# Kernel optimization log

Hardware: AMD Instinct MI355X
Metric: run time of the kernel (lower is better)

Reference implementation:

```python
import jax, jax.numpy as jnp
import numpy as np

ALPHA = 0.1  # label smoothing coefficient

def setup_inputs() -> dict:
    key = jax.random.key(0)
    k1, k2, k3 = jax.random.split(key, 3)
    B, T, V = 8, 512, 8192
    inputs = jax.random.normal(k1, (B, T, V), dtype=jnp.float32)
    # token ids in [2, V); last position of every sample is EOS (id 1)
    body = jax.random.randint(k2, (B, T), 2, V)
    targets = body.at[:, -1].set(1)
    matric = jax.random.uniform(k3, (V, V), dtype=jnp.float32)  # confusion matrix
    label_lengths = jnp.full((B,), T - 1, dtype=jnp.int32)  # len(label); target adds EOS
    return {"inputs": inputs, "matric": matric, "targets": targets,
            "label_lengths": label_lengths}


def reference(inputs, matric, targets, label_lengths):
    B, T, V = inputs.shape
    x = inputs.reshape(-1, V)          # [N, V]
    t = targets.reshape(-1)            # [N]
    N = x.shape[0]

    # --- segment-wise confusion lookup (vectorized over ragged segments) ---
    eos = (t == 1)
    # row index for each token: previous token in its segment, or N-1 at a
    # segment start (faithful to `targets.shape[-1]-1` in the source).
    prev = jnp.roll(t, 1)
    is_start = jnp.roll(eos, 1).at[0].set(True)
    forth = jnp.where(is_start, N - 1, prev)
    need_smoothed = matric[forth, t]   # [N]

    # --- per-segment smoothing coefficient, broadcast to tokens ---
    length = label_lengths + 1                                   # [B]
    sm = 1.0 - jnp.power(1.0 - ALPHA, 1.0 / length.astype(jnp.float32))  # [B]
    eos_i = eos.astype(jnp.int32)
    seg_id = jnp.cumsum(eos_i) - eos_i                           # [N] segment index
    smoothing = sm[seg_id] * need_smoothed                       # [N]

    # --- smoothed target distribution ---
    off = smoothing / (V - 1)                                    # off-target mass
    src = 1.0 - off * V                                          # 1 - weight.sum(1)
    weight = jnp.broadcast_to(off[:, None], (N, V))
    weight = weight.at[jnp.arange(N), t].set(src)

    # --- KLDiv(log_softmax(x), weight), reduction='none', then sum/len ---
    logp = jax.nn.log_softmax(x, axis=1)
    kl = jax.scipy.special.xlogy(weight, weight) - weight * logp
    return kl.sum() / length.sum()
```

## Files before the change

kernel.cpp:

```cpp
#include <hip/hip_runtime.h>
#include <math.h>

#define ALPHA 0.1f

__global__ __launch_bounds__(256) void token_params_kernel(
    const int* __restrict__ t, const float* __restrict__ matric,
    const int* __restrict__ lens, float* __restrict__ offv,
    float* __restrict__ srcv, float* __restrict__ lensum,
    int N, int V, int B)
{
    __shared__ int cnts[256];
    const int tid = threadIdx.x;
    const int chunk = (N + 255) / 256;
    const int c0 = tid * chunk;
    const int c1 = min(c0 + chunk, N);

    int cnt = 0;
    for (int n = c0; n < c1; ++n) cnt += (t[n] == 1);
    cnts[tid] = cnt;
    __syncthreads();

    for (int d = 1; d < 256; d <<= 1) {
        int v = 0;
        if (tid >= d) v = cnts[tid - d];
        __syncthreads();
        if (tid >= d) cnts[tid] += v;
        __syncthreads();
    }
    int run = (tid == 0) ? 0 : cnts[tid - 1];

    const float inv_vm1 = 1.0f / (float)(V - 1);
    for (int n = c0; n < c1; ++n) {
        const int tn = t[n];
        const bool e = (tn == 1);
        int seg = run;
        if (e) run += 1;
        seg = min(seg, B - 1);
        if (seg < 0) seg = 0;

        const int prev = (n == 0) ? 0 : t[n - 1];
        const bool is_start = (n == 0) || (prev == 1);
        const int forth = is_start ? (N - 1) : prev;

        const float need = matric[(size_t)forth * V + tn];
        const float len = (float)(lens[seg] + 1);
        const float sm = 1.0f - powf(1.0f - ALPHA, 1.0f / len);
        const float off = sm * need * inv_vm1;
        offv[n] = off;
        srcv[n] = 1.0f - off * (float)V;
    }

    if (tid == 0) {
        float ls = 0.f;
        for (int b = 0; b < B; ++b) ls += (float)(lens[b] + 1);
        lensum[0] = ls;
    }
}

__device__ __forceinline__ void combine_ms(float& m, float& s, float om, float os) {
    float nm = fmaxf(m, om);
    s = s * __expf(m - nm) + os * __expf(om - nm);
    m = nm;
}

__device__ __forceinline__ void row_epilogue(
    float M, float Z, float Sx, float xt,
    const float* __restrict__ offv, const float* __restrict__ srcv,
    float* __restrict__ rowkl, int row, int V)
{
    const float logZ = logf(Z) + M;
    const float lpt = xt - logZ;
    const float S = Sx - (float)V * logZ;
    const float o = offv[row];
    const float sr = srcv[row];
    const float xlo = (o > 0.f) ? o * logf(o) : 0.f;
    const float xls = (sr > 0.f) ? sr * logf(sr) : 0.f;
    rowkl[row] = (float)(V - 1) * xlo + xls - (o * (S - lpt) + sr * lpt);
}

template <int NV4>
__global__ __launch_bounds__(256) void row_kl_kernel(
    const float* __restrict__ x, const int* __restrict__ t,
    const float* __restrict__ offv, const float* __restrict__ srcv,
    float* __restrict__ rowkl, int V)
{
    const int row = blockIdx.x;
    const int tid = threadIdx.x;
    const float4* xr = reinterpret_cast<const float4*>(x + (size_t)row * V);

    float4 v[NV4];
#pragma unroll
    for (int k = 0; k < NV4; ++k) v[k] = xr[tid + k * 256];

    const int tgt = t[row];
    float m = -INFINITY, sx = 0.f, xt_local = 0.f;
    bool have = false;
#pragma unroll
    for (int k = 0; k < NV4; ++k) {
        const float4 q = v[k];
        m = fmaxf(fmaxf(fmaxf(m, q.x), q.y), fmaxf(q.z, q.w));
        sx += (q.x + q.y) + (q.z + q.w);
        const int c = tgt - 4 * (tid + k * 256);
        if (c >= 0 && c < 4) {
            xt_local = (c == 0) ? q.x : (c == 1) ? q.y : (c == 2) ? q.z : q.w;
            have = true;
        }
    }
    float s = 0.f;
#pragma unroll
    for (int k = 0; k < NV4; ++k) {
        const float4 q = v[k];
        s += (__expf(q.x - m) + __expf(q.y - m)) + (__expf(q.z - m) + __expf(q.w - m));
    }

    __shared__ float sm_m[4], sm_s[4], sm_sx[4], sm_xt;
    if (have) sm_xt = xt_local;

    for (int d = 1; d < 64; d <<= 1) {
        float om = __shfl_xor(m, d);
        float os = __shfl_xor(s, d);
        float osx = __shfl_xor(sx, d);
        combine_ms(m, s, om, os);
        sx += osx;
    }
    const int lane = tid & 63, wid = tid >> 6;
    if (lane == 0) { sm_m[wid] = m; sm_s[wid] = s; sm_sx[wid] = sx; }
    __syncthreads();
    if (tid == 0) {
        for (int w = 1; w < 4; ++w) { combine_ms(m, s, sm_m[w], sm_s[w]); sx += sm_sx[w]; }
        row_epilogue(m, s, sx, sm_xt, offv, srcv, rowkl, row, V);
    }
}

__global__ __launch_bounds__(256) void row_kl_generic(
    const float* __restrict__ x, const int* __restrict__ t,
    const float* __restrict__ offv, const float* __restrict__ srcv,
    float* __restrict__ rowkl, int V)
{
    const int row = blockIdx.x;
    const int tid = threadIdx.x;
    const float* xr = x + (size_t)row * V;
    const int tgt = t[row];

    float m = -INFINITY, sx = 0.f, xt = 0.f;
    bool have = false;
    for (int i = tid; i < V; i += 256) {
        const float q = xr[i];
        m = fmaxf(m, q);
        sx += q;
        if (i == tgt) { xt = q; have = true; }
    }
    __shared__ float shm[4], shs[4], shsx[4], shxt, shM;
    if (have) shxt = xt;
    for (int d = 1; d < 64; d <<= 1) {
        m = fmaxf(m, __shfl_xor(m, d));
        sx += __shfl_xor(sx, d);
    }
    const int lane = tid & 63, wid = tid >> 6;
    if (lane == 0) { shm[wid] = m; shsx[wid] = sx; }
    __syncthreads();
    if (tid == 0) {
        float M = shm[0];
        for (int w = 1; w < 4; ++w) M = fmaxf(M, shm[w]);
        shM = M;
    }
    __syncthreads();
    const float M = shM;
    float s = 0.f;
    for (int i = tid; i < V; i += 256) s += __expf(xr[i] - M);
    for (int d = 1; d < 64; d <<= 1) s += __shfl_xor(s, d);
    if (lane == 0) shs[wid] = s;
    __syncthreads();
    if (tid == 0) {
        const float Z = shs[0] + shs[1] + shs[2] + shs[3];
        const float SX = shsx[0] + shsx[1] + shsx[2] + shsx[3];
        row_epilogue(M, Z, SX, shxt, offv, srcv, rowkl, row, V);
    }
}

__global__ __launch_bounds__(256) void finalize_kernel(
    const float* __restrict__ rowkl, const float* __restrict__ lensum,
    float* __restrict__ out, int N)
{
    __shared__ float sh[4];
    float a = 0.f;
    for (int i = threadIdx.x; i < N; i += 256) a += rowkl[i];
    for (int d = 1; d < 64; d <<= 1) a += __shfl_xor(a, d);
    const int lane = threadIdx.x & 63, wid = threadIdx.x >> 6;
    if (lane == 0) sh[wid] = a;
    __syncthreads();
    if (threadIdx.x == 0) {
        out[0] = (sh[0] + sh[1] + sh[2] + sh[3]) / lensum[0];
    }
}

extern "C" void kernel_launch(void* const* d_in, const int* in_sizes, int n_in,
                              void* d_out, int out_size, void* d_ws, size_t ws_size,
                              hipStream_t stream) {
    const float* x      = (const float*)d_in[0];
    const float* matric = (const float*)d_in[1];
    const int*   tgts   = (const int*)d_in[2];
    const int*   lens   = (const int*)d_in[3];

    const int N = in_sizes[2];
    const int B = in_sizes[3];
    const int V = in_sizes[0] / in_sizes[2];

    float* ws     = (float*)d_ws;
    float* rowkl  = ws;
    float* offv   = ws + N;
    float* srcv   = ws + 2 * N;
    float* lensum = ws + 3 * N;

    token_params_kernel<<<1, 256, 0, stream>>>(tgts, matric, lens, offv, srcv,
                                               lensum, N, V, B);
    if (V == 8 * 256 * 4) {
        row_kl_kernel<8><<<N, 256, 0, stream>>>(x, tgts, offv, srcv, rowkl, V);
    } else {
        row_kl_generic<<<N, 256, 0, stream>>>(x, tgts, offv, srcv, rowkl, V);
    }
    finalize_kernel<<<1, 256, 0, stream>>>(rowkl, lensum, (float*)d_out, N);
}
```

Measured before the change: 400.6 us.

## Fuse per-token parameter computation and final reduction into row KL kernel

For the specialized vocabulary size, the single-block token-parameter kernel and the finalize kernel are removed. Each row block now counts EOS tokens before its row to find its segment, looks up the confusion entry itself, and atomically adds its scaled KL term to the output, which a one-thread kernel zeroes first. This removes a serial one-block kernel and a reduction launch. In exchange every block rescans up to N targets (a quadratic amount of small reads overall) and the atomic float sum has nondeterministic ordering.

After: 396.5 us. Within noise of the previous version (-1.0%).

```diff
diff --git a/kernel.cpp b/kernel.cpp
--- a/kernel.cpp
+++ b/kernel.cpp
@@ -3,58 +3,8 @@
 
 #define ALPHA 0.1f
 
-__global__ __launch_bounds__(256) void token_params_kernel(
-    const int* __restrict__ t, const float* __restrict__ matric,
-    const int* __restrict__ lens, float* __restrict__ offv,
-    float* __restrict__ srcv, float* __restrict__ lensum,
-    int N, int V, int B)
-{
-    __shared__ int cnts[256];
-    const int tid = threadIdx.x;
-    const int chunk = (N + 255) / 256;
-    const int c0 = tid * chunk;
-    const int c1 = min(c0 + chunk, N);
-
-    int cnt = 0;
-    for (int n = c0; n < c1; ++n) cnt += (t[n] == 1);
-    cnts[tid] = cnt;
-    __syncthreads();
-
-    for (int d = 1; d < 256; d <<= 1) {
-        int v = 0;
-        if (tid >= d) v = cnts[tid - d];
-        __syncthreads();
-        if (tid >= d) cnts[tid] += v;
-        __syncthreads();
-    }
-    int run = (tid == 0) ? 0 : cnts[tid - 1];
-
-    const float inv_vm1 = 1.0f / (float)(V - 1);
-    for (int n = c0; n < c1; ++n) {
-        const int tn = t[n];
-        const bool e = (tn == 1);
-        int seg = run;
-        if (e) run += 1;
-        seg = min(seg, B - 1);
-        if (seg < 0) seg = 0;
-
-        const int prev = (n == 0) ? 0 : t[n - 1];
-        const bool is_start = (n == 0) || (prev == 1);
-        const int forth = is_start ? (N - 1) : prev;
-
-        const float need = matric[(size_t)forth * V + tn];
-        const float len = (float)(lens[seg] + 1);
-        const float sm = 1.0f - powf(1.0f - ALPHA, 1.0f / len);
-        const float off = sm * need * inv_vm1;
-        offv[n] = off;
-        srcv[n] = 1.0f - off * (float)V;
-    }
-
-    if (tid == 0) {
-        float ls = 0.f;
-        for (int b = 0; b < B; ++b) ls += (float)(lens[b] + 1);
-        lensum[0] = ls;
-    }
+__global__ void zero_out_kernel(float* __restrict__ out) {
+    out[0] = 0.0f;
 }
 
 __device__ __forceinline__ void combine_ms(float& m, float& s, float om, float os) {
@@ -63,34 +13,48 @@
     m = nm;
 }
 
-__device__ __forceinline__ void row_epilogue(
-    float M, float Z, float Sx, float xt,
-    const float* __restrict__ offv, const float* __restrict__ srcv,
-    float* __restrict__ rowkl, int row, int V)
-{
-    const float logZ = logf(Z) + M;
-    const float lpt = xt - logZ;
-    const float S = Sx - (float)V * logZ;
-    const float o = offv[row];
-    const float sr = srcv[row];
-    const float xlo = (o > 0.f) ? o * logf(o) : 0.f;
-    const float xls = (sr > 0.f) ? sr * logf(sr) : 0.f;
-    rowkl[row] = (float)(V - 1) * xlo + xls - (o * (S - lpt) + sr * lpt);
-}
-
 template <int NV4>
-__global__ __launch_bounds__(256) void row_kl_kernel(
-    const float* __restrict__ x, const int* __restrict__ t,
-    const float* __restrict__ offv, const float* __restrict__ srcv,
-    float* __restrict__ rowkl, int V)
+__global__ __launch_bounds__(256) void fused_row_kl(
+    const float* __restrict__ x, const float* __restrict__ matric,
+    const int* __restrict__ t, const int* __restrict__ lens,
+    float* __restrict__ out, int N, int V, int B)
 {
     const int row = blockIdx.x;
     const int tid = threadIdx.x;
+
     const float4* xr = reinterpret_cast<const float4*>(x + (size_t)row * V);
-
     float4 v[NV4];
 #pragma unroll
     for (int k = 0; k < NV4; ++k) v[k] = xr[tid + k * 256];
+
+    int cnt = 0;
+    for (int i = tid; i < row; i += 256) cnt += (t[i] == 1);
+    for (int d = 1; d < 64; d <<= 1) cnt += __shfl_xor(cnt, d);
+
+    __shared__ int scnt[4];
+    __shared__ float sh_off, sh_src, sh_ls, sh_xt;
+    __shared__ float sm_m[4], sm_s[4], sm_sx[4];
+    const int lane = tid & 63, wid = tid >> 6;
+    if (lane == 0) scnt[wid] = cnt;
+    __syncthreads();
+
+    if (tid == 0) {
+        int seg = scnt[0] + scnt[1] + scnt[2] + scnt[3];
+        seg = min(max(seg, 0), B - 1);
+        const int tn = t[row];
+        const int prev = (row == 0) ? 0 : t[row - 1];
+        const bool is_start = (row == 0) || (prev == 1);
+        const int forth = is_start ? (N - 1) : prev;
+        const float need = matric[(size_t)forth * V + tn];
+        const float len = (float)(lens[seg] + 1);
+        const float sm = 1.0f - powf(1.0f - ALPHA, 1.0f / len);
+        const float off = sm * need / (float)(V - 1);
+        sh_off = off;
+        sh_src = 1.0f - off * (float)V;
+        float ls = 0.f;
+        for (int b = 0; b < B; ++b) ls += (float)(lens[b] + 1);
+        sh_ls = ls;
+    }
 
     const int tgt = t[row];
     float m = -INFINITY, sx = 0.f, xt_local = 0.f;
@@ -106,15 +70,14 @@
             have = true;
         }
     }
+    if (have) sh_xt = xt_local;
+
     float s = 0.f;
 #pragma unroll
     for (int k = 0; k < NV4; ++k) {
         const float4 q = v[k];
         s += (__expf(q.x - m) + __expf(q.y - m)) + (__expf(q.z - m) + __expf(q.w - m));
     }
-
-    __shared__ float sm_m[4], sm_s[4], sm_sx[4], sm_xt;
-    if (have) sm_xt = xt_local;
 
     for (int d = 1; d < 64; d <<= 1) {
         float om = __shfl_xor(m, d);
@@ -123,12 +86,67 @@
         combine_ms(m, s, om, os);
         sx += osx;
     }
-    const int lane = tid & 63, wid = tid >> 6;
     if (lane == 0) { sm_m[wid] = m; sm_s[wid] = s; sm_sx[wid] = sx; }
     __syncthreads();
+
     if (tid == 0) {
         for (int w = 1; w < 4; ++w) { combine_ms(m, s, sm_m[w], sm_s[w]); sx += sm_sx[w]; }
-        row_epilogue(m, s, sx, sm_xt, offv, srcv, rowkl, row, V);
+        const float logZ = logf(s) + m;
+        const float lpt = sh_xt - logZ;
+        const float S = sx - (float)V * logZ;
+        const float o = sh_off;
+        const float sr = sh_src;
+        const float xlo = (o > 0.f) ? o * logf(o) : 0.f;
+        const float xls = (sr > 0.f) ? sr * logf(sr) : 0.f;
+        const float kl = (float)(V - 1) * xlo + xls - (o * (S - lpt) + sr * lpt);
+        atomicAdd(out, kl / sh_ls);
+    }
+}
+
+__global__ __launch_bounds__(256) void token_params_kernel(
+    const int* __restrict__ t, const float* __restrict__ matric,
+    const int* __restrict__ lens, float* __restrict__ offv,
+    float* __restrict__ srcv, float* __restrict__ lensum,
+    int N, int V, int B)
+{
+    __shared__ int cnts[256];
+    const int tid = threadIdx.x;
+    const int chunk = (N + 255) / 256;
+    const int c0 = tid * chunk;
+    const int c1 = min(c0 + chunk, N);
+
+    int cnt = 0;
+    for (int n = c0; n < c1; ++n) cnt += (t[n] == 1);
+    cnts[tid] = cnt;
+    __syncthreads();
+    for (int d = 1; d < 256; d <<= 1) {
+        int v = 0;
+        if (tid >= d) v = cnts[tid - d];
+        __syncthreads();
+        if (tid >= d) cnts[tid] += v;
+        __syncthreads();
+    }
+    int run = (tid == 0) ? 0 : cnts[tid - 1];
+
+    const float inv_vm1 = 1.0f / (float)(V - 1);
+    for (int n = c0; n < c1; ++n) {
+        const int tn = t[n];
+        int seg = min(max(run, 0), B - 1);
+        if (tn == 1) run += 1;
+        const int prev = (n == 0) ? 0 : t[n - 1];
+        const bool is_start = (n == 0) || (prev == 1);
+        const int forth = is_start ? (N - 1) : prev;
+        const float need = matric[(size_t)forth * V + tn];
+        const float len = (float)(lens[seg] + 1);
+        const float sm = 1.0f - powf(1.0f - ALPHA, 1.0f / len);
+        const float off = sm * need * inv_vm1;
+        offv[n] = off;
+        srcv[n] = 1.0f - off * (float)V;
+    }
+    if (tid == 0) {
+        float ls = 0.f;
+        for (int b = 0; b < B; ++b) ls += (float)(lens[b] + 1);
+        lensum[0] = ls;
     }
 }
 
@@ -174,7 +192,14 @@
     if (tid == 0) {
         const float Z = shs[0] + shs[1] + shs[2] + shs[3];
         const float SX = shsx[0] + shsx[1] + shsx[2] + shsx[3];
-        row_epilogue(M, Z, SX, shxt, offv, srcv, rowkl, row, V);
+        const float logZ = logf(Z) + M;
+        const float lpt = shxt - logZ;
+        const float S = SX - (float)V * logZ;
+        const float o = offv[row];
+        const float sr = srcv[row];
+        const float xlo = (o > 0.f) ? o * logf(o) : 0.f;
+        const float xls = (sr > 0.f) ? sr * logf(sr) : 0.f;
+        rowkl[row] = (float)(V - 1) * xlo + xls - (o * (S - lpt) + sr * lpt);
     }
 }
 
@@ -206,18 +231,19 @@
     const int B = in_sizes[3];
     const int V = in_sizes[0] / in_sizes[2];
 
-    float* ws     = (float*)d_ws;
-    float* rowkl  = ws;
-    float* offv   = ws + N;
-    float* srcv   = ws + 2 * N;
-    float* lensum = ws + 3 * N;
-
-    token_params_kernel<<<1, 256, 0, stream>>>(tgts, matric, lens, offv, srcv,
-                                               lensum, N, V, B);
     if (V == 8 * 256 * 4) {
-        row_kl_kernel<8><<<N, 256, 0, stream>>>(x, tgts, offv, srcv, rowkl, V);
+        zero_out_kernel<<<1, 1, 0, stream>>>((float*)d_out);
+        fused_row_kl<8><<<N, 256, 0, stream>>>(x, matric, tgts, lens,
+                                               (float*)d_out, N, V, B);
     } else {
+        float* ws     = (float*)d_ws;
+        float* rowkl  = ws;
+        float* offv   = ws + N;
+        float* srcv   = ws + 2 * N;
+        float* lensum = ws + 3 * N;
+        token_params_kernel<<<1, 256, 0, stream>>>(tgts, matric, lens, offv, srcv,
+                                                   lensum, N, V, B);
         row_kl_generic<<<N, 256, 0, stream>>>(x, tgts, offv, srcv, rowkl, V);
-    }
-    finalize_kernel<<<1, 256, 0, stream>>>(rowkl, lensum, (float*)d_out, N);
-}
+        finalize_kernel<<<1, 256, 0, stream>>>(rowkl, lensum, (float*)d_out, N);
+    }
+}
```
